# Kernel tuning notes

Hardware: AMD Instinct MI355X
Metric: run time of the kernel (lower is better)

## Reference

```python
import jax, jax.numpy as jnp
import numpy as np

EPS = 1e-5

def gelu(x):
    return jax.nn.gelu(x, approximate=False)

def conv1x1(x, w, b):
    # x: [B,C,H,W], w: [O,C], b: [O]
    return jnp.einsum('bchw,oc->bohw', x, w) + b[None, :, None, None]

def dwconv3(x, w, b):
    # depthwise 3x3, w: [C,1,3,3]
    C = x.shape[1]
    y = jax.lax.conv_general_dilated(x, w, (1, 1), 'SAME',
                                     feature_group_count=C,
                                     dimension_numbers=('NCHW', 'OIHW', 'NCHW'))
    return y + b[None, :, None, None]

def groupnorm(x, g, b):
    # GroupNorm(1, C): normalize over (C,H,W) per sample, per-channel affine
    m = x.mean(axis=(1, 2, 3), keepdims=True)
    v = x.var(axis=(1, 2, 3), keepdims=True)
    xn = (x - m) * jax.lax.rsqrt(v + EPS)
    return xn * g[None, :, None, None] + b[None, :, None, None]

@jax.custom_vjp
def spike(u):
    return (u > 0.0).astype(u.dtype)

def _spike_fwd(u):
    return spike(u), u

def _spike_bwd(u, g):
    # rectangular surrogate gradient of width 0.5 around the threshold
    return (g * (jnp.abs(u) < 0.5).astype(g.dtype),)

spike.defvjp(_spike_fwd, _spike_bwd)

def lif_along(x, tau, vth, axis):
    # leaky-integrate-fire recurrence along `axis` (H or W) treated as time
    xt = jnp.moveaxis(x, axis, 0)  # [T, ...]
    z = jnp.zeros_like(xt[0])
    def step(carry, x_t):
        u_prev, o_prev = carry
        u = x_t + tau * u_prev * (1.0 - o_prev)  # hard reset on spike
        o = spike(u - vth)
        return (u, o), o
    _, out = jax.lax.scan(step, (z, z), xt)
    return jnp.moveaxis(out, 0, axis)


def setup_inputs() -> dict:
    key = jax.random.key(0)
    ks = jax.random.split(key, 8)
    B, C, H, W = 64, 96, 56, 56
    Hd = 4 * C
    def w(k, shape, s=0.02):
        return jax.random.normal(k, shape, jnp.float32) * s
    f32 = jnp.float32
    return dict(
        x=jax.random.normal(ks[0], (B, C, H, W), f32),
        n1g=jnp.ones(C, f32), n1b=jnp.zeros(C, f32),
        c1w=w(ks[1], (C, C)), c1b=jnp.zeros(C, f32),
        g1g=jnp.ones(C, f32), g1b=jnp.zeros(C, f32),
        dww=w(ks[2], (C, 1, 3, 3)), dwb=jnp.zeros(C, f32),
        g2g=jnp.ones(C, f32), g2b=jnp.zeros(C, f32),
        tau1=jnp.array(0.25, f32), vth1=jnp.array(-1.0, f32),
        tau2=jnp.array(0.25, f32), vth2=jnp.array(-1.0, f32),
        c21w=w(ks[3], (C, C)), c21b=jnp.zeros(C, f32),
        c22w=w(ks[4], (C, C)), c22b=jnp.zeros(C, f32),
        g3g=jnp.ones(C, f32), g3b=jnp.zeros(C, f32),
        c3w=w(ks[5], (C, C)), c3b=jnp.zeros(C, f32),
        n2g=jnp.ones(C, f32), n2b=jnp.zeros(C, f32),
        f1w=w(ks[6], (Hd, C)), f1b=jnp.zeros(Hd, f32),
        f2w=w(ks[7], (C, Hd)), f2b=jnp.zeros(C, f32),
    )


def reference(x, n1g, n1b, c1w, c1b, g1g, g1b, dww, dwb, g2g, g2b,
              tau1, vth1, tau2, vth2, c21w, c21b, c22w, c22b,
              g3g, g3b, c3w, c3b, n2g, n2b, f1w, f1b, f2w, f2b):
    shortcut = x
    # LIF module
    h = groupnorm(x, n1g, n1b)                               # block norm1 (MyNorm)
    h = gelu(groupnorm(conv1x1(h, c1w, c1b), g1g, g1b))      # conv1 -> norm1 -> GELU
    h = gelu(groupnorm(dwconv3(h, dww, dwb), g2g, g2b))      # dw1 -> norm2 -> GELU
    x_lr = lif_along(h, tau1, vth1, axis=2)                  # LIF over H
    x_td = lif_along(h, tau2, vth2, axis=3)                  # LIF over W
    h = gelu(conv1x1(x_lr, c21w, c21b)) + gelu(conv1x1(x_td, c22w, c22b))
    h = conv1x1(groupnorm(h, g3g, g3b), c3w, c3b)            # norm3 -> conv3
    x = shortcut + h
    # MLP branch (1x1 convs)
    m = groupnorm(x, n2g, n2b)
    m = conv1x1(gelu(conv1x1(m, f1w, f1b)), f2w, f2b)
    return x + m
```

## Files before the change

kernel.cpp:

```cpp
#include <hip/hip_runtime.h>

#define BB 64
#define CC 96
#define HH 56
#define WW 56
#define HWSZ (HH*WW)
#define CHW (CC*HWSZ)
#define NTOT ((size_t)BB*CHW)
#define S_SPLIT 32
#define CHUNK (CHW/S_SPLIT)
#define HD 384
#define NP 104

typedef float f32x4  __attribute__((ext_vector_type(4)));
typedef short bf16x8 __attribute__((ext_vector_type(8)));
typedef unsigned short u16x4 __attribute__((ext_vector_type(4)));

__device__ __forceinline__ unsigned short f2bf(float f) {
    unsigned int u = __float_as_uint(f);
    u = (u + 0x7FFFu + ((u >> 16) & 1u)) >> 16;
    return (unsigned short)u;
}
__device__ __forceinline__ float bf2f(unsigned short u) {
    return __uint_as_float(((unsigned int)u) << 16);
}
__device__ __forceinline__ float gelu_t(float x) {
    float s = x*x;
    float q = __builtin_fmaf(s, 0.102943f, 2.3021953f) * x;
    float t = exp2f(q);
    float r = __builtin_amdgcn_rcpf(1.0f + t);
    return __builtin_fmaf(-x, r, x);
}
__device__ __forceinline__ bf16x8 ldfrag(const unsigned short* p) {
    return *reinterpret_cast<const bf16x8*>(p);
}

__global__ __launch_bounds__(256) void wconv(const float* __restrict__ c1w, const float* __restrict__ c21w,
        const float* __restrict__ c22w, const float* __restrict__ c3w,
        const float* __restrict__ f1w, const float* __restrict__ f2w,
        unsigned short* __restrict__ wbf) {
    int i = blockIdx.x*256 + threadIdx.x;
    int blk = i / 9216;
    int idx = i - blk*9216;
    int tm   = idx / 1536;
    int rem  = idx - tm*1536;
    int ks   = rem / 512;
    int rem2 = rem - ks*512;
    int lane = rem2 >> 3;
    int j    = rem2 & 7;
    int row = tm*16 + (lane & 15);
    int col = ks*32 + (lane >> 4)*8 + j;
    float v;
    if      (blk == 0) v = c1w [row*CC + col];
    else if (blk == 1) v = c21w[row*CC + col];
    else if (blk == 2) v = c22w[row*CC + col];
    else if (blk == 3) v = c3w [row*CC + col];
    else if (blk <  8) v = f1w[((blk-4)*CC + row)*CC + col];
    else               v = f2w[row*HD + (blk-8)*CC + col];
    wbf[i] = f2bf(v);
}

__global__ __launch_bounds__(256) void gn_partial(const float* __restrict__ in, float2* __restrict__ part) {
    int b = blockIdx.y, s = blockIdx.x;
    const float* p = in + (size_t)b*CHW + (size_t)s*CHUNK;
    float sum = 0.f, sq = 0.f;
    for (int i = threadIdx.x; i < CHUNK; i += 256) {
        float v = p[i];
        sum += v; sq += v*v;
    }
    for (int off = 32; off > 0; off >>= 1) {
        sum += __shfl_down(sum, off);
        sq  += __shfl_down(sq,  off);
    }
    __shared__ float2 red[4];
    int wid = threadIdx.x >> 6, lane = threadIdx.x & 63;
    if (lane == 0) red[wid] = make_float2(sum, sq);
    __syncthreads();
    if (threadIdx.x == 0) {
        for (int i = 1; i < 4; i++) { sum += red[i].x; sq += red[i].y; }
        part[b*S_SPLIT + s] = make_float2(sum, sq);
    }
}

template<int NPART>
__global__ void gn_final(const float2* __restrict__ part, float2* __restrict__ stats) {
    int b = threadIdx.x;
    if (b >= BB) return;
    float s = 0.f, q = 0.f;
    for (int i = 0; i < NPART; i++) { float2 v = part[b*NPART + i]; s += v.x; q += v.y; }
    float mean = s / (float)CHW;
    float var  = q / (float)CHW - mean*mean;
    stats[b] = make_float2(mean, rsqrtf(var + 1e-5f));
}

template<bool IN_BF, bool OUT_RES>
__global__ __launch_bounds__(256) void convk(const void* __restrict__ in_,
        const unsigned short* __restrict__ wbf, const float* __restrict__ bias,
        const float2* __restrict__ st_in, const float* __restrict__ gam, const float* __restrict__ bet,
        const float* __restrict__ res, void* __restrict__ out_, float2* __restrict__ part) {
    __shared__ unsigned short xs[128][NP];
    __shared__ float gml[CC], btl[CC];
    __shared__ float2 red[8];
    int tid = threadIdx.x;
    int b0 = blockIdx.y, b1 = b0 + 32;
    int hw0 = blockIdx.x * 64;
    if (tid < CC) { gml[tid] = gam[tid]; btl[tid] = bet[tid]; }
    float2 st0 = st_in[b0], st1 = st_in[b1];
    __syncthreads();
    int col = tid & 63;
    for (int c4 = (tid >> 6)*4; c4 < CC; c4 += 16) {
        unsigned int pk0[2], pk1[2];
        #pragma unroll
        for (int j = 0; j < 4; j++) {
            int c = c4 + j;
            size_t off0 = (size_t)b0*CHW + (size_t)c*HWSZ + hw0 + col;
            size_t off1 = (size_t)b1*CHW + (size_t)c*HWSZ + hw0 + col;
            float r0 = IN_BF ? bf2f(((const unsigned short*)in_)[off0]) : ((const float*)in_)[off0];
            float r1 = IN_BF ? bf2f(((const unsigned short*)in_)[off1]) : ((const float*)in_)[off1];
            float a0 = st0.y * gml[c], b0c = __builtin_fmaf(-st0.x, a0, btl[c]);
            float a1 = st1.y * gml[c], b1c = __builtin_fmaf(-st1.x, a1, btl[c]);
            unsigned short h0 = f2bf(__builtin_fmaf(r0, a0, b0c));
            unsigned short h1 = f2bf(__builtin_fmaf(r1, a1, b1c));
            if (j < 2) { if (j == 0) { pk0[0] = h0; pk1[0] = h1; } else { pk0[0] |= (unsigned int)h0 << 16; pk1[0] |= (unsigned int)h1 << 16; } }
            else       { if (j == 2) { pk0[1] = h0; pk1[1] = h1; } else { pk0[1] |= (unsigned int)h0 << 16; pk1[1] |= (unsigned int)h1 << 16; } }
        }
        *reinterpret_cast<uint2*>(&xs[col][c4])      = make_uint2(pk0[0], pk0[1]);
        *reinterpret_cast<uint2*>(&xs[64+col][c4])   = make_uint2(pk1[0], pk1[1]);
    }
    __syncthreads();
    int lane = tid & 63, wid = tid >> 6;
    int ln = lane & 15, k0 = (lane >> 4)*8, n0 = wid*16;
    const unsigned short* wl = wbf + lane*8;
    f32x4 a0[6], a1[6];
    #pragma unroll
    for (int t = 0; t < 6; t++) { a0[t] = (f32x4){0,0,0,0}; a1[t] = (f32x4){0,0,0,0}; }
    #pragma unroll
    for (int ks = 0; ks < 3; ks++) {
        bf16x8 bf0 = ldfrag(&xs[n0+ln][ks*32+k0]);
        bf16x8 bf1 = ldfrag(&xs[64+n0+ln][ks*32+k0]);
        #pragma unroll
        for (int tm = 0; tm < 6; tm++) {
            bf16x8 af = ldfrag(wl + (tm*3+ks)*512);
            a0[tm] = __builtin_amdgcn_mfma_f32_16x16x32_bf16(af, bf0, a0[tm], 0, 0, 0);
            a1[tm] = __builtin_amdgcn_mfma_f32_16x16x32_bf16(af, bf1, a1[tm], 0, 0, 0);
        }
    }
    int r0i = (lane >> 4)*4;
    size_t ob0 = (size_t)b0*CHW + hw0 + n0 + ln;
    size_t ob1 = (size_t)b1*CHW + hw0 + n0 + ln;
    float s0 = 0.f, q0 = 0.f, s1 = 0.f, q1 = 0.f;
    #pragma unroll
    for (int tm = 0; tm < 6; tm++) {
        #pragma unroll
        for (int r = 0; r < 4; r++) {
            int o = tm*16 + r0i + r;
            size_t i0 = ob0 + (size_t)o*HWSZ, i1 = ob1 + (size_t)o*HWSZ;
            float v0 = a0[tm][r] + bias[o];
            float v1 = a1[tm][r] + bias[o];
            if (OUT_RES) { v0 += res[i0]; v1 += res[i1];
                           ((float*)out_)[i0] = v0; ((float*)out_)[i1] = v1; }
            else         { ((unsigned short*)out_)[i0] = f2bf(v0); ((unsigned short*)out_)[i1] = f2bf(v1); }
            s0 += v0; q0 += v0*v0; s1 += v1; q1 += v1*v1;
        }
    }
    for (int off = 32; off > 0; off >>= 1) {
        s0 += __shfl_down(s0, off); q0 += __shfl_down(q0, off);
        s1 += __shfl_down(s1, off); q1 += __shfl_down(q1, off);
    }
    if (lane == 0) { red[wid] = make_float2(s0, q0); red[4+wid] = make_float2(s1, q1); }
    __syncthreads();
    if (tid == 0) {
        float S0=0,Q0=0,S1=0,Q1=0;
        for (int i = 0; i < 4; i++) { S0 += red[i].x; Q0 += red[i].y; S1 += red[4+i].x; Q1 += red[4+i].y; }
        part[b0*49 + blockIdx.x] = make_float2(S0, Q0);
        part[b1*49 + blockIdx.x] = make_float2(S1, Q1);
    }
}

__global__ __launch_bounds__(256) void dw_fused(const unsigned short* __restrict__ t1,
        const float* __restrict__ dww, const float* __restrict__ dwb,
        const float2* __restrict__ st_in, const float* __restrict__ gam, const float* __restrict__ bet,
        unsigned short* __restrict__ t2, float2* __restrict__ part) {
    __shared__ float tile[HH*57];
    __shared__ float2 red[4];
    int bc = blockIdx.x;
    int b = bc / CC, c = bc - b*CC;
    int tid = threadIdx.x;
    float2 st = st_in[b];
    float ga = gam[c]*st.y;
    float bb = __builtin_fmaf(-st.x, ga, bet[c]);
    const unsigned short* ip = t1 + (size_t)bc*HWSZ;
    for (int i = tid; i < HWSZ; i += 256) {
        float v = __builtin_fmaf(bf2f(ip[i]), ga, bb);
        tile[(i/WW)*57 + (i%WW)] = gelu_t(v);
    }
    __syncthreads();
    float w00=dww[c*9+0],w01=dww[c*9+1],w02=dww[c*9+2],
          w10=dww[c*9+3],w11=dww[c*9+4],w12=dww[c*9+5],
          w20=dww[c*9+6],w21=dww[c*9+7],w22=dww[c*9+8];
    float bs = dwb[c];
    unsigned short* op = t2 + (size_t)bc*HWSZ;
    float s = 0.f, q = 0.f;
    for (int i = tid; i < HWSZ; i += 256) {
        int h = i/WW, w_ = i - h*WW;
        float acc = bs;
        int up = h > 0, dn = h < HH-1, lf = w_ > 0, rt = w_ < WW-1;
        const float* rm = &tile[(h-1)*57 + w_];
        const float* r0p = &tile[h*57 + w_];
        const float* rp = &tile[(h+1)*57 + w_];
        if (up) { if (lf) acc += rm[-1]*w00; acc += rm[0]*w01; if (rt) acc += rm[1]*w02; }
        if (lf) acc += r0p[-1]*w10;
        acc += r0p[0]*w11;
        if (rt) acc += r0p[1]*w12;
        if (dn) { if (lf) acc += rp[-1]*w20; acc += rp[0]*w21; if (rt) acc += rp[1]*w22; }
        op[i] = f2bf(acc);
        s += acc; q += acc*acc;
    }
    for (int off = 32; off > 0; off >>= 1) { s += __shfl_down(s, off); q += __shfl_down(q, off); }
    int wid = tid >> 6, lane = tid & 63;
    if (lane == 0) red[wid] = make_float2(s, q);
    __syncthreads();
    if (tid == 0) {
        for (int i = 1; i < 4; i++) { s += red[i].x; q += red[i].y; }
        part[bc] = make_float2(s, q);
    }
}

__global__ __launch_bounds__(64) void lif_hw(const unsigned short* __restrict__ t2,
        unsigned short* __restrict__ xlr, unsigned short* __restrict__ xtd,
        const float2* __restrict__ st_in, const float* __restrict__ gam, const float* __restrict__ bet,
        const float* __restrict__ tau1p, const float* __restrict__ vth1p,
        const float* __restrict__ tau2p, const float* __restrict__ vth2p) {
    __shared__ float tile[HH*57];
    int bc = blockIdx.x;
    int b = bc / CC, c = bc - b*CC;
    int tid = threadIdx.x;
    float2 st = st_in[b];
    float ga = gam[c]*st.y;
    float bb = __builtin_fmaf(-st.x, ga, bet[c]);
    const unsigned short* ip = t2 + (size_t)bc*HWSZ;
    for (int i = tid; i < HWSZ/4; i += 64) {
        u16x4 v = *reinterpret_cast<const u16x4*>(ip + i*4);
        int h = i / 14;
        int w0 = (i - h*14)*4;
        float* tp = &tile[h*57 + w0];
        #pragma unroll
        for (int j = 0; j < 4; j++)
            tp[j] = gelu_t(__builtin_fmaf(bf2f((unsigned short)v[j]), ga, bb));
    }
    __syncthreads();
    const float tau1 = *tau1p, vth1 = *vth1p;
    if (tid < WW) {
        float u = 0.f, o = 0.f;
        unsigned short* op = xlr + (size_t)bc*HWSZ + tid;
        for (int h = 0; h < HH; h++) {
            float xv = tile[h*57 + tid];
            u = xv + tau1*u*(1.f - o);
            o = (u - vth1 > 0.f) ? 1.f : 0.f;
            op[h*WW] = (o != 0.f) ? (unsigned short)0x3F80 : (unsigned short)0;
        }
    }
    __syncthreads();
    const float tau2 = *tau2p, vth2 = *vth2p;
    if (tid < HH) {
        float u = 0.f, o = 0.f;
        int off = tid*57;
        for (int w_ = 0; w_ < WW; w_++) {
            float xv = tile[off + w_];
            u = xv + tau2*u*(1.f - o);
            o = (u - vth2 > 0.f) ? 1.f : 0.f;
            tile[off + w_] = o;
        }
    }
    __syncthreads();
    unsigned int* op32 = (unsigned int*)(xtd + (size_t)bc*HWSZ);
    for (int i = tid; i < HWSZ/2; i += 64) {
        int h = i / 28;
        int w0 = (i - h*28)*2;
        unsigned int lo = tile[h*57 + w0]     != 0.f ? 0x3F80u : 0u;
        unsigned int hi = tile[h*57 + w0 + 1] != 0.f ? 0x3F80u : 0u;
        op32[i] = lo | (hi << 16);
    }
}

__global__ __launch_bounds__(256) void dual_mfma(const unsigned short* __restrict__ xa_g, const unsigned short* __restrict__ xb_g,
        const unsigned short* __restrict__ w1bf, const float* __restrict__ b1,
        const unsigned short* __restrict__ w2bf, const float* __restrict__ b2,
        unsigned short* __restrict__ out, float2* __restrict__ part) {
    __shared__ unsigned short xa[64][NP];
    __shared__ unsigned short xb[64][NP];
    __shared__ float2 red[4];
    int tid = threadIdx.x;
    int b = blockIdx.y;
    int hw0 = blockIdx.x * 64;
    int col = tid & 63;
    const unsigned short* ap = xa_g + (size_t)b*CHW + hw0 + col;
    const unsigned short* bp = xb_g + (size_t)b*CHW + hw0 + col;
    for (int c4 = (tid >> 6)*4; c4 < CC; c4 += 16) {
        unsigned int pa0, pa1, pb0, pb1;
        unsigned short a0 = ap[(size_t)(c4+0)*HWSZ], a1v = ap[(size_t)(c4+1)*HWSZ];
        unsigned short a2 = ap[(size_t)(c4+2)*HWSZ], a3 = ap[(size_t)(c4+3)*HWSZ];
        unsigned short b0v = bp[(size_t)(c4+0)*HWSZ], b1v = bp[(size_t)(c4+1)*HWSZ];
        unsigned short b2v = bp[(size_t)(c4+2)*HWSZ], b3v = bp[(size_t)(c4+3)*HWSZ];
        pa0 = (unsigned int)a0 | ((unsigned int)a1v << 16);
        pa1 = (unsigned int)a2 | ((unsigned int)a3 << 16);
        pb0 = (unsigned int)b0v | ((unsigned int)b1v << 16);
        pb1 = (unsigned int)b2v | ((unsigned int)b3v << 16);
        *reinterpret_cast<uint2*>(&xa[col][c4]) = make_uint2(pa0, pa1);
        *reinterpret_cast<uint2*>(&xb[col][c4]) = make_uint2(pb0, pb1);
    }
    __syncthreads();
    int lane = tid & 63, wid = tid >> 6;
    int ln = lane & 15, k0 = (lane >> 4)*8, n0 = wid*16;
    const unsigned short* wl1 = w1bf + lane*8;
    const unsigned short* wl2 = w2bf + lane*8;
    f32x4 acc1[6], acc2[6];
    #pragma unroll
    for (int t = 0; t < 6; t++) { acc1[t] = (f32x4){0,0,0,0}; acc2[t] = (f32x4){0,0,0,0}; }
    #pragma unroll
    for (int ks = 0; ks < 3; ks++) {
        bf16x8 bfa = ldfrag(&xa[n0+ln][ks*32+k0]);
        bf16x8 bfb = ldfrag(&xb[n0+ln][ks*32+k0]);
        #pragma unroll
        for (int tm = 0; tm < 6; tm++) {
            bf16x8 af1 = ldfrag(wl1 + (tm*3+ks)*512);
            bf16x8 af2 = ldfrag(wl2 + (tm*3+ks)*512);
            acc1[tm] = __builtin_amdgcn_mfma_f32_16x16x32_bf16(af1, bfa, acc1[tm], 0, 0, 0);
            acc2[tm] = __builtin_amdgcn_mfma_f32_16x16x32_bf16(af2, bfb, acc2[tm], 0, 0, 0);
        }
    }
    int r0i = (lane >> 4)*4;
    size_t ob = (size_t)b*CHW + hw0 + n0 + ln;
    float s = 0.f, q = 0.f;
    #pragma unroll
    for (int tm = 0; tm < 6; tm++) {
        #pragma unroll
        for (int r = 0; r < 4; r++) {
            int o = tm*16 + r0i + r;
            float v = gelu_t(acc1[tm][r] + b1[o]) + gelu_t(acc2[tm][r] + b2[o]);
            out[ob + (size_t)o*HWSZ] = f2bf(v);
            s += v; q += v*v;
        }
    }
    for (int off = 32; off > 0; off >>= 1) { s += __shfl_down(s, off); q += __shfl_down(q, off); }
    if (lane == 0) red[wid] = make_float2(s, q);
    __syncthreads();
    if (tid == 0) {
        for (int i = 1; i < 4; i++) { s += red[i].x; q += red[i].y; }
        part[b*49 + blockIdx.x] = make_float2(s, q);
    }
}

__global__ __launch_bounds__(512, 4) void mlp_mfma(float* __restrict__ xio, const float2* __restrict__ st_in,
        const float* __restrict__ gam, const float* __restrict__ bet,
        const unsigned short* __restrict__ wbf, const float* __restrict__ b1, const float* __restrict__ b2) {
    __shared__ unsigned short xs[128][NP];
    __shared__ unsigned short mc[128][NP];
    __shared__ float gml[CC], btl[CC];
    int tid = threadIdx.x;
    int b0 = blockIdx.y, b1i = b0 + 32;
    int hw0 = blockIdx.x * 64;
    if (tid < CC) { gml[tid] = gam[tid]; btl[tid] = bet[tid]; }
    float2 st0 = st_in[b0], st1 = st_in[b1i];
    __syncthreads();
    {
        int col = tid & 63;
        int bsel0 = (tid >> 6) & 1;
        float2 st = bsel0 ? st1 : st0;
        size_t base = (size_t)(bsel0 ? b1i : b0)*CHW + hw0 + col;
        for (int c4 = (tid >> 7)*4; c4 < CC; c4 += 16) {
            unsigned int pk[2];
            #pragma unroll
            for (int j = 0; j < 4; j++) {
                int c = c4 + j;
                float rv = xio[base + (size_t)c*HWSZ];
                float a = st.y * gml[c];
                float bc = __builtin_fmaf(-st.x, a, btl[c]);
                unsigned short h = f2bf(__builtin_fmaf(rv, a, bc));
                if (j < 2) { if (j == 0) pk[0] = h; else pk[0] |= (unsigned int)h << 16; }
                else       { if (j == 2) pk[1] = h; else pk[1] |= (unsigned int)h << 16; }
            }
            *reinterpret_cast<uint2*>(&xs[bsel0*64 + col][c4]) = make_uint2(pk[0], pk[1]);
        }
    }
    __syncthreads();
    int lane = tid & 63, wv = tid >> 6;
    int mh = wv >> 2;
    int cg = wv & 3;
    int ln = lane & 15, k0 = (lane >> 4)*8;
    int r0i = (lane >> 4)*4;
    int xrow0 = cg*32 + ln;
    int xrow1 = xrow0 + 16;
    f32x4 ao[3][2];
    #pragma unroll
    for (int t = 0; t < 3; t++) { ao[t][0] = (f32x4){0,0,0,0}; ao[t][1] = (f32x4){0,0,0,0}; }
    for (int ch = 0; ch < 4; ch++) {
        const unsigned short* w1l = wbf + (4+ch)*9216 + mh*4608 + lane*8;
        const unsigned short* w2l = wbf + (8+ch)*9216 + mh*4608 + lane*8;
        f32x4 c1[3][2];
        #pragma unroll
        for (int t = 0; t < 3; t++) { c1[t][0] = (f32x4){0,0,0,0}; c1[t][1] = (f32x4){0,0,0,0}; }
        __builtin_amdgcn_s_setprio(1);
        #pragma unroll
        for (int ks = 0; ks < 3; ks++) {
            bf16x8 bfa = ldfrag(&xs[xrow0][ks*32+k0]);
            bf16x8 bfb = ldfrag(&xs[xrow1][ks*32+k0]);
            #pragma unroll
            for (int tm = 0; tm < 3; tm++) {
                bf16x8 af = ldfrag(w1l + (tm*3+ks)*512);
                c1[tm][0] = __builtin_amdgcn_mfma_f32_16x16x32_bf16(af, bfa, c1[tm][0], 0, 0, 0);
                c1[tm][1] = __builtin_amdgcn_mfma_f32_16x16x32_bf16(af, bfb, c1[tm][1], 0, 0, 0);
            }
        }
        __builtin_amdgcn_s_setprio(0);
        #pragma unroll
        for (int tm = 0; tm < 3; tm++) {
            int d0 = mh*48 + tm*16 + r0i;
            int dch = ch*CC + d0;
            unsigned short m0 = f2bf(gelu_t(c1[tm][0][0] + b1[dch+0]));
            unsigned short m1 = f2bf(gelu_t(c1[tm][0][1] + b1[dch+1]));
            unsigned short m2 = f2bf(gelu_t(c1[tm][0][2] + b1[dch+2]));
            unsigned short m3 = f2bf(gelu_t(c1[tm][0][3] + b1[dch+3]));
            *reinterpret_cast<uint2*>(&mc[xrow0][d0]) =
                make_uint2((unsigned int)m0 | ((unsigned int)m1 << 16),
                           (unsigned int)m2 | ((unsigned int)m3 << 16));
            unsigned short n0v = f2bf(gelu_t(c1[tm][1][0] + b1[dch+0]));
            unsigned short n1v = f2bf(gelu_t(c1[tm][1][1] + b1[dch+1]));
            unsigned short n2v = f2bf(gelu_t(c1[tm][1][2] + b1[dch+2]));
            unsigned short n3v = f2bf(gelu_t(c1[tm][1][3] + b1[dch+3]));
            *reinterpret_cast<uint2*>(&mc[xrow1][d0]) =
                make_uint2((unsigned int)n0v | ((unsigned int)n1v << 16),
                           (unsigned int)n2v | ((unsigned int)n3v << 16));
        }
        __syncthreads();
        __builtin_amdgcn_s_setprio(1);
        #pragma unroll
        for (int ks = 0; ks < 3; ks++) {
            bf16x8 bfa = ldfrag(&mc[xrow0][ks*32+k0]);
            bf16x8 bfb = ldfrag(&mc[xrow1][ks*32+k0]);
            #pragma unroll
            for (int tm = 0; tm < 3; tm++) {
                bf16x8 af = ldfrag(w2l + (tm*3+ks)*512);
                ao[tm][0] = __builtin_amdgcn_mfma_f32_16x16x32_bf16(af, bfa, ao[tm][0], 0, 0, 0);
                ao[tm][1] = __builtin_amdgcn_mfma_f32_16x16x32_bf16(af, bfb, ao[tm][1], 0, 0, 0);
            }
        }
        __builtin_amdgcn_s_setprio(0);
        __syncthreads();
    }
    int bsel = cg >> 1;
    size_t ob = (size_t)(bsel ? b1i : b0)*CHW + hw0 + (cg & 1)*32 + ln;
    #pragma unroll
    for (int tm = 0; tm < 3; tm++) {
        #pragma unroll
        for (int r = 0; r < 4; r++) {
            int o = mh*48 + tm*16 + r0i + r;
            size_t i0 = ob + (size_t)o*HWSZ;
            float bo = b2[o];
            xio[i0]      = xio[i0]      + bo + ao[tm][0][r];
            xio[i0 + 16] = xio[i0 + 16] + bo + ao[tm][1][r];
        }
    }
}

extern "C" void kernel_launch(void* const* d_in, const int* in_sizes, int n_in,
                              void* d_out, int out_size, void* d_ws, size_t ws_size,
                              hipStream_t stream) {
    (void)in_sizes; (void)n_in; (void)out_size; (void)ws_size;
    const float* x    = (const float*)d_in[0];
    const float* n1g  = (const float*)d_in[1];
    const float* n1b  = (const float*)d_in[2];
    const float* c1w  = (const float*)d_in[3];
    const float* c1b  = (const float*)d_in[4];
    const float* g1g  = (const float*)d_in[5];
    const float* g1b  = (const float*)d_in[6];
    const float* dww  = (const float*)d_in[7];
    const float* dwb  = (const float*)d_in[8];
    const float* g2g  = (const float*)d_in[9];
    const float* g2b  = (const float*)d_in[10];
    const float* tau1 = (const float*)d_in[11];
    const float* vth1 = (const float*)d_in[12];
    const float* tau2 = (const float*)d_in[13];
    const float* vth2 = (const float*)d_in[14];
    const float* c21w = (const float*)d_in[15];
    const float* c21b = (const float*)d_in[16];
    const float* c22w = (const float*)d_in[17];
    const float* c22b = (const float*)d_in[18];
    const float* g3g  = (const float*)d_in[19];
    const float* g3b  = (const float*)d_in[20];
    const float* c3w  = (const float*)d_in[21];
    const float* c3b  = (const float*)d_in[22];
    const float* n2g  = (const float*)d_in[23];
    const float* n2b  = (const float*)d_in[24];
    const float* f1w  = (const float*)d_in[25];
    const float* f1b  = (const float*)d_in[26];
    const float* f2w  = (const float*)d_in[27];
    const float* f2b  = (const float*)d_in[28];
    float* out = (float*)d_out;

    unsigned short* A   = (unsigned short*)d_ws;
    unsigned short* Bb  = A  + NTOT;
    unsigned short* Cc  = Bb + NTOT;
    unsigned short* WBF = Cc + NTOT;
    float2* part  = (float2*)(WBF + 110592);
    float2* stats = part + 64*96;
    float2* s_n1 = stats, * s_g1 = stats+64, * s_g2 = stats+128, * s_g3 = stats+192, * s_n2 = stats+256;

    const unsigned short* Wc1  = WBF;
    const unsigned short* Wc21 = WBF + 9216;
    const unsigned short* Wc22 = WBF + 18432;
    const unsigned short* Wc3  = WBF + 27648;

    dim3 gStat(S_SPLIT, BB);
    dim3 gPair(HWSZ/64, BB/2);
    dim3 gSing(HWSZ/64, BB);

    wconv<<<432,256,0,stream>>>(c1w, c21w, c22w, c3w, f1w, f2w, WBF);
    gn_partial<<<gStat,256,0,stream>>>(x, part);
    gn_final<S_SPLIT><<<1,64,0,stream>>>(part, s_n1);
    convk<false,false><<<gPair,256,0,stream>>>(x, Wc1, c1b, s_n1, n1g, n1b, nullptr, A, part);
    gn_final<49><<<1,64,0,stream>>>(part, s_g1);
    dw_fused<<<BB*CC,256,0,stream>>>(A, dww, dwb, s_g1, g1g, g1b, Bb, part);
    gn_final<CC><<<1,64,0,stream>>>(part, s_g2);
    lif_hw<<<BB*CC,64,0,stream>>>(Bb, A, Cc, s_g2, g2g, g2b, tau1, vth1, tau2, vth2);
    dual_mfma<<<gSing,256,0,stream>>>(A, Cc, Wc21, c21b, Wc22, c22b, Bb, part);
    gn_final<49><<<1,64,0,stream>>>(part, s_g3);
    convk<true,true><<<gPair,256,0,stream>>>(Bb, Wc3, c3b, s_g3, g3g, g3b, x, out, part);
    gn_final<49><<<1,64,0,stream>>>(part, s_n2);
    mlp_mfma<<<gPair,512,0,stream>>>(out, s_n2, n2g, n2b, WBF, f1b, f2b);
}
```

Before: 319.8 us.

## Fold groupnorm finalization into consumer kernels and rebalance MFMA wave tiling

```diff
diff --git a/kernel.cpp b/kernel.cpp
--- a/kernel.cpp
+++ b/kernel.cpp
@@ -33,6 +33,24 @@
 }
 __device__ __forceinline__ bf16x8 ldfrag(const unsigned short* p) {
     return *reinterpret_cast<const bf16x8*>(p);
+}
+template<int NPART>
+__device__ __forceinline__ float2 stats_from_parts(const float2* __restrict__ part, int b) {
+    int lane = threadIdx.x & 63;
+    float s = 0.f, q = 0.f;
+    for (int i = lane; i < NPART; i += 64) {
+        float2 v = part[b*NPART + i];
+        s += v.x; q += v.y;
+    }
+    #pragma unroll
+    for (int off = 32; off > 0; off >>= 1) {
+        s += __shfl_down(s, off);
+        q += __shfl_down(q, off);
+    }
+    s = __shfl(s, 0); q = __shfl(q, 0);
+    float mean = s / (float)CHW;
+    float var  = q / (float)CHW - mean*mean;
+    return make_float2(mean, rsqrtf(var + 1e-5f));
 }
 
 __global__ __launch_bounds__(256) void wconv(const float* __restrict__ c1w, const float* __restrict__ c21w,
@@ -62,12 +80,14 @@
 
 __global__ __launch_bounds__(256) void gn_partial(const float* __restrict__ in, float2* __restrict__ part) {
     int b = blockIdx.y, s = blockIdx.x;
-    const float* p = in + (size_t)b*CHW + (size_t)s*CHUNK;
+    const float4* p = (const float4*)(in + (size_t)b*CHW + (size_t)s*CHUNK);
     float sum = 0.f, sq = 0.f;
-    for (int i = threadIdx.x; i < CHUNK; i += 256) {
-        float v = p[i];
-        sum += v; sq += v*v;
-    }
+    for (int i = threadIdx.x; i < CHUNK/4; i += 256) {
+        float4 v = p[i];
+        sum += v.x+v.y+v.z+v.w;
+        sq  += v.x*v.x+v.y*v.y+v.z*v.z+v.w*v.w;
+    }
+    #pragma unroll
     for (int off = 32; off > 0; off >>= 1) {
         sum += __shfl_down(sum, off);
         sq  += __shfl_down(sq,  off);
@@ -82,30 +102,20 @@
     }
 }
 
-template<int NPART>
-__global__ void gn_final(const float2* __restrict__ part, float2* __restrict__ stats) {
-    int b = threadIdx.x;
-    if (b >= BB) return;
-    float s = 0.f, q = 0.f;
-    for (int i = 0; i < NPART; i++) { float2 v = part[b*NPART + i]; s += v.x; q += v.y; }
-    float mean = s / (float)CHW;
-    float var  = q / (float)CHW - mean*mean;
-    stats[b] = make_float2(mean, rsqrtf(var + 1e-5f));
-}
-
-template<bool IN_BF, bool OUT_RES>
+template<bool IN_BF, bool OUT_RES, int NPART>
 __global__ __launch_bounds__(256) void convk(const void* __restrict__ in_,
         const unsigned short* __restrict__ wbf, const float* __restrict__ bias,
-        const float2* __restrict__ st_in, const float* __restrict__ gam, const float* __restrict__ bet,
-        const float* __restrict__ res, void* __restrict__ out_, float2* __restrict__ part) {
+        const float2* __restrict__ part_in, const float* __restrict__ gam, const float* __restrict__ bet,
+        const float* __restrict__ res, void* __restrict__ out_, float2* __restrict__ part_out) {
     __shared__ unsigned short xs[128][NP];
     __shared__ float gml[CC], btl[CC];
-    __shared__ float2 red[8];
+    __shared__ float2 red[4];
     int tid = threadIdx.x;
     int b0 = blockIdx.y, b1 = b0 + 32;
     int hw0 = blockIdx.x * 64;
+    float2 st0 = stats_from_parts<NPART>(part_in, b0);
+    float2 st1 = stats_from_parts<NPART>(part_in, b1);
     if (tid < CC) { gml[tid] = gam[tid]; btl[tid] = bet[tid]; }
-    float2 st0 = st_in[b0], st1 = st_in[b1];
     __syncthreads();
     int col = tid & 63;
     for (int c4 = (tid >> 6)*4; c4 < CC; c4 += 16) {
@@ -128,65 +138,67 @@
         *reinterpret_cast<uint2*>(&xs[64+col][c4])   = make_uint2(pk1[0], pk1[1]);
     }
     __syncthreads();
-    int lane = tid & 63, wid = tid >> 6;
-    int ln = lane & 15, k0 = (lane >> 4)*8, n0 = wid*16;
-    const unsigned short* wl = wbf + lane*8;
-    f32x4 a0[6], a1[6];
-    #pragma unroll
-    for (int t = 0; t < 6; t++) { a0[t] = (f32x4){0,0,0,0}; a1[t] = (f32x4){0,0,0,0}; }
+    int lane = tid & 63, wv = tid >> 6;
+    int mh = wv >> 1, cg = wv & 1;
+    int ln = lane & 15, k0 = (lane >> 4)*8, r0i = (lane >> 4)*4;
+    const unsigned short* wl = wbf + mh*4608 + lane*8;
+    f32x4 acc[3][4];
+    #pragma unroll
+    for (int t = 0; t < 3; t++)
+        #pragma unroll
+        for (int x = 0; x < 4; x++) acc[t][x] = (f32x4){0,0,0,0};
+    __builtin_amdgcn_s_setprio(1);
     #pragma unroll
     for (int ks = 0; ks < 3; ks++) {
-        bf16x8 bf0 = ldfrag(&xs[n0+ln][ks*32+k0]);
-        bf16x8 bf1 = ldfrag(&xs[64+n0+ln][ks*32+k0]);
-        #pragma unroll
-        for (int tm = 0; tm < 6; tm++) {
+        bf16x8 bfr[4];
+        #pragma unroll
+        for (int xr = 0; xr < 4; xr++) bfr[xr] = ldfrag(&xs[cg*64 + xr*16 + ln][ks*32+k0]);
+        #pragma unroll
+        for (int tm = 0; tm < 3; tm++) {
             bf16x8 af = ldfrag(wl + (tm*3+ks)*512);
-            a0[tm] = __builtin_amdgcn_mfma_f32_16x16x32_bf16(af, bf0, a0[tm], 0, 0, 0);
-            a1[tm] = __builtin_amdgcn_mfma_f32_16x16x32_bf16(af, bf1, a1[tm], 0, 0, 0);
-        }
-    }
-    int r0i = (lane >> 4)*4;
-    size_t ob0 = (size_t)b0*CHW + hw0 + n0 + ln;
-    size_t ob1 = (size_t)b1*CHW + hw0 + n0 + ln;
-    float s0 = 0.f, q0 = 0.f, s1 = 0.f, q1 = 0.f;
-    #pragma unroll
-    for (int tm = 0; tm < 6; tm++) {
-        #pragma unroll
-        for (int r = 0; r < 4; r++) {
-            int o = tm*16 + r0i + r;
-            size_t i0 = ob0 + (size_t)o*HWSZ, i1 = ob1 + (size_t)o*HWSZ;
-            float v0 = a0[tm][r] + bias[o];
-            float v1 = a1[tm][r] + bias[o];
-            if (OUT_RES) { v0 += res[i0]; v1 += res[i1];
-                           ((float*)out_)[i0] = v0; ((float*)out_)[i1] = v1; }
-            else         { ((unsigned short*)out_)[i0] = f2bf(v0); ((unsigned short*)out_)[i1] = f2bf(v1); }
-            s0 += v0; q0 += v0*v0; s1 += v1; q1 += v1*v1;
-        }
-    }
-    for (int off = 32; off > 0; off >>= 1) {
-        s0 += __shfl_down(s0, off); q0 += __shfl_down(q0, off);
-        s1 += __shfl_down(s1, off); q1 += __shfl_down(q1, off);
-    }
-    if (lane == 0) { red[wid] = make_float2(s0, q0); red[4+wid] = make_float2(s1, q1); }
+            #pragma unroll
+            for (int xr = 0; xr < 4; xr++)
+                acc[tm][xr] = __builtin_amdgcn_mfma_f32_16x16x32_bf16(af, bfr[xr], acc[tm][xr], 0, 0, 0);
+        }
+    }
+    __builtin_amdgcn_s_setprio(0);
+    size_t obase = (size_t)(cg ? b1 : b0)*CHW + hw0;
+    float s = 0.f, q = 0.f;
+    #pragma unroll
+    for (int tm = 0; tm < 3; tm++) {
+        #pragma unroll
+        for (int xr = 0; xr < 4; xr++) {
+            #pragma unroll
+            for (int r = 0; r < 4; r++) {
+                int o = mh*48 + tm*16 + r0i + r;
+                size_t idx = obase + (size_t)o*HWSZ + xr*16 + ln;
+                float v = acc[tm][xr][r] + bias[o];
+                if (OUT_RES) { v += res[idx]; ((float*)out_)[idx] = v; }
+                else         { ((unsigned short*)out_)[idx] = f2bf(v); }
+                s += v; q += v*v;
+            }
+        }
+    }
+    #pragma unroll
+    for (int off = 32; off > 0; off >>= 1) { s += __shfl_down(s, off); q += __shfl_down(q, off); }
+    if (lane == 0) red[wv] = make_float2(s, q);
     __syncthreads();
     if (tid == 0) {
-        float S0=0,Q0=0,S1=0,Q1=0;
-        for (int i = 0; i < 4; i++) { S0 += red[i].x; Q0 += red[i].y; S1 += red[4+i].x; Q1 += red[4+i].y; }
-        part[b0*49 + blockIdx.x] = make_float2(S0, Q0);
-        part[b1*49 + blockIdx.x] = make_float2(S1, Q1);
+        part_out[b0*49 + blockIdx.x] = make_float2(red[0].x + red[2].x, red[0].y + red[2].y);
+        part_out[b1*49 + blockIdx.x] = make_float2(red[1].x + red[3].x, red[1].y + red[3].y);
     }
 }
 
 __global__ __launch_bounds__(256) void dw_fused(const unsigned short* __restrict__ t1,
         const float* __restrict__ dww, const float* __restrict__ dwb,
-        const float2* __restrict__ st_in, const float* __restrict__ gam, const float* __restrict__ bet,
-        unsigned short* __restrict__ t2, float2* __restrict__ part) {
+        const float2* __restrict__ part_in, const float* __restrict__ gam, const float* __restrict__ bet,
+        unsigned short* __restrict__ t2, float2* __restrict__ part_out) {
     __shared__ float tile[HH*57];
     __shared__ float2 red[4];
     int bc = blockIdx.x;
     int b = bc / CC, c = bc - b*CC;
     int tid = threadIdx.x;
-    float2 st = st_in[b];
+    float2 st = stats_from_parts<49>(part_in, b);
     float ga = gam[c]*st.y;
     float bb = __builtin_fmaf(-st.x, ga, bet[c]);
     const unsigned short* ip = t1 + (size_t)bc*HWSZ;
@@ -216,26 +228,27 @@
         op[i] = f2bf(acc);
         s += acc; q += acc*acc;
     }
+    #pragma unroll
     for (int off = 32; off > 0; off >>= 1) { s += __shfl_down(s, off); q += __shfl_down(q, off); }
     int wid = tid >> 6, lane = tid & 63;
     if (lane == 0) red[wid] = make_float2(s, q);
     __syncthreads();
     if (tid == 0) {
         for (int i = 1; i < 4; i++) { s += red[i].x; q += red[i].y; }
-        part[bc] = make_float2(s, q);
+        part_out[bc] = make_float2(s, q);
     }
 }
 
 __global__ __launch_bounds__(64) void lif_hw(const unsigned short* __restrict__ t2,
         unsigned short* __restrict__ xlr, unsigned short* __restrict__ xtd,
-        const float2* __restrict__ st_in, const float* __restrict__ gam, const float* __restrict__ bet,
+        const float2* __restrict__ part_in, const float* __restrict__ gam, const float* __restrict__ bet,
         const float* __restrict__ tau1p, const float* __restrict__ vth1p,
         const float* __restrict__ tau2p, const float* __restrict__ vth2p) {
     __shared__ float tile[HH*57];
     int bc = blockIdx.x;
     int b = bc / CC, c = bc - b*CC;
     int tid = threadIdx.x;
-    float2 st = st_in[b];
+    float2 st = stats_from_parts<96>(part_in, b);
     float ga = gam[c]*st.y;
     float bb = __builtin_fmaf(-st.x, ga, bet[c]);
     const unsigned short* ip = t2 + (size_t)bc*HWSZ;
@@ -286,7 +299,7 @@
 __global__ __launch_bounds__(256) void dual_mfma(const unsigned short* __restrict__ xa_g, const unsigned short* __restrict__ xb_g,
         const unsigned short* __restrict__ w1bf, const float* __restrict__ b1,
         const unsigned short* __restrict__ w2bf, const float* __restrict__ b2,
-        unsigned short* __restrict__ out, float2* __restrict__ part) {
+        unsigned short* __restrict__ out, float2* __restrict__ part_out) {
     __shared__ unsigned short xa[64][NP];
     __shared__ unsigned short xb[64][NP];
     __shared__ float2 red[4];
@@ -297,72 +310,80 @@
     const unsigned short* ap = xa_g + (size_t)b*CHW + hw0 + col;
     const unsigned short* bp = xb_g + (size_t)b*CHW + hw0 + col;
     for (int c4 = (tid >> 6)*4; c4 < CC; c4 += 16) {
-        unsigned int pa0, pa1, pb0, pb1;
         unsigned short a0 = ap[(size_t)(c4+0)*HWSZ], a1v = ap[(size_t)(c4+1)*HWSZ];
         unsigned short a2 = ap[(size_t)(c4+2)*HWSZ], a3 = ap[(size_t)(c4+3)*HWSZ];
         unsigned short b0v = bp[(size_t)(c4+0)*HWSZ], b1v = bp[(size_t)(c4+1)*HWSZ];
         unsigned short b2v = bp[(size_t)(c4+2)*HWSZ], b3v = bp[(size_t)(c4+3)*HWSZ];
-        pa0 = (unsigned int)a0 | ((unsigned int)a1v << 16);
-        pa1 = (unsigned int)a2 | ((unsigned int)a3 << 16);
-        pb0 = (unsigned int)b0v | ((unsigned int)b1v << 16);
-        pb1 = (unsigned int)b2v | ((unsigned int)b3v << 16);
-        *reinterpret_cast<uint2*>(&xa[col][c4]) = make_uint2(pa0, pa1);
-        *reinterpret_cast<uint2*>(&xb[col][c4]) = make_uint2(pb0, pb1);
-    }
-    __syncthreads();
-    int lane = tid & 63, wid = tid >> 6;
-    int ln = lane & 15, k0 = (lane >> 4)*8, n0 = wid*16;
-    const unsigned short* wl1 = w1bf + lane*8;
-    const unsigned short* wl2 = w2bf + lane*8;
-    f32x4 acc1[6], acc2[6];
-    #pragma unroll
-    for (int t = 0; t < 6; t++) { acc1[t] = (f32x4){0,0,0,0}; acc2[t] = (f32x4){0,0,0,0}; }
+        *reinterpret_cast<uint2*>(&xa[col][c4]) =
+            make_uint2((unsigned int)a0 | ((unsigned int)a1v << 16), (unsigned int)a2 | ((unsigned int)a3 << 16));
+        *reinterpret_cast<uint2*>(&xb[col][c4]) =
+            make_uint2((unsigned int)b0v | ((unsigned int)b1v << 16), (unsigned int)b2v | ((unsigned int)b3v << 16));
+    }
+    __syncthreads();
+    int lane = tid & 63, wv = tid >> 6;
+    int mh = wv >> 1, cg = wv & 1;
+    int ln = lane & 15, k0 = (lane >> 4)*8, r0i = (lane >> 4)*4;
+    const unsigned short* wl1 = w1bf + mh*4608 + lane*8;
+    const unsigned short* wl2 = w2bf + mh*4608 + lane*8;
+    f32x4 acc1[3][2], acc2[3][2];
+    #pragma unroll
+    for (int t = 0; t < 3; t++) {
+        acc1[t][0] = (f32x4){0,0,0,0}; acc1[t][1] = (f32x4){0,0,0,0};
+        acc2[t][0] = (f32x4){0,0,0,0}; acc2[t][1] = (f32x4){0,0,0,0};
+    }
+    __builtin_amdgcn_s_setprio(1);
     #pragma unroll
     for (int ks = 0; ks < 3; ks++) {
-        bf16x8 bfa = ldfrag(&xa[n0+ln][ks*32+k0]);
-        bf16x8 bfb = ldfrag(&xb[n0+ln][ks*32+k0]);
-        #pragma unroll
-        for (int tm = 0; tm < 6; tm++) {
+        bf16x8 bfa0 = ldfrag(&xa[cg*32 + ln][ks*32+k0]);
+        bf16x8 bfa1 = ldfrag(&xa[cg*32 + 16 + ln][ks*32+k0]);
+        bf16x8 bfb0 = ldfrag(&xb[cg*32 + ln][ks*32+k0]);
+        bf16x8 bfb1 = ldfrag(&xb[cg*32 + 16 + ln][ks*32+k0]);
+        #pragma unroll
+        for (int tm = 0; tm < 3; tm++) {
             bf16x8 af1 = ldfrag(wl1 + (tm*3+ks)*512);
             bf16x8 af2 = ldfrag(wl2 + (tm*3+ks)*512);
-            acc1[tm] = __builtin_amdgcn_mfma_f32_16x16x32_bf16(af1, bfa, acc1[tm], 0, 0, 0);
-            acc2[tm] = __builtin_amdgcn_mfma_f32_16x16x32_bf16(af2, bfb, acc2[tm], 0, 0, 0);
-        }
-    }
-    int r0i = (lane >> 4)*4;
-    size_t ob = (size_t)b*CHW + hw0 + n0 + ln;
+            acc1[tm][0] = __builtin_amdgcn_mfma_f32_16x16x32_bf16(af1, bfa0, acc1[tm][0], 0, 0, 0);
+            acc1[tm][1] = __builtin_amdgcn_mfma_f32_16x16x32_bf16(af1, bfa1, acc1[tm][1], 0, 0, 0);
+            acc2[tm][0] = __builtin_amdgcn_mfma_f32_16x16x32_bf16(af2, bfb0, acc2[tm][0], 0, 0, 0);
+            acc2[tm][1] = __builtin_amdgcn_mfma_f32_16x16x32_bf16(af2, bfb1, acc2[tm][1], 0, 0, 0);
+        }
+    }
+    __builtin_amdgcn_s_setprio(0);
+    size_t ob = (size_t)b*CHW + hw0;
     float s = 0.f, q = 0.f;
     #pragma unroll
-    for (int tm = 0; tm < 6; tm++) {
-        #pragma unroll
-        for (int r = 0; r < 4; r++) {
-            int o = tm*16 + r0i + r;
-            float v = gelu_t(acc1[tm][r] + b1[o]) + gelu_t(acc2[tm][r] + b2[o]);
-            out[ob + (size_t)o*HWSZ] = f2bf(v);
-            s += v; q += v*v;
-        }
-    }
+    for (int tm = 0; tm < 3; tm++) {
+        #pragma unroll
+        for (int xr = 0; xr < 2; xr++) {
+            #pragma unroll
+            for (int r = 0; r < 4; r++) {
+                int o = mh*48 + tm*16 + r0i + r;
+                float v = gelu_t(acc1[tm][xr][r] + b1[o]) + gelu_t(acc2[tm][xr][r] + b2[o]);
+                out[ob + (size_t)o*HWSZ + cg*32 + xr*16 + ln] = f2bf(v);
+                s += v; q += v*v;
+            }
+        }
+    }
+    #pragma unroll
     for (int off = 32; off > 0; off >>= 1) { s += __shfl_down(s, off); q += __shfl_down(q, off); }
-    if (lane == 0) red[wid] = make_float2(s, q);
+    if (lane == 0) red[wv] = make_float2(s, q);
     __syncthreads();
     if (tid == 0) {
         for (int i = 1; i < 4; i++) { s += red[i].x; q += red[i].y; }
-        part[b*49 + blockIdx.x] = make_float2(s, q);
-    }
-}
-
-__global__ __launch_bounds__(512, 4) void mlp_mfma(float* __restrict__ xio, const float2* __restrict__ st_in,
+        part_out[b*49 + blockIdx.x] = make_float2(s, q);
+    }
+}
+
+__global__ __launch_bounds__(512, 6) void mlp_mfma(float* __restrict__ xio, const float2* __restrict__ part_in,
         const float* __restrict__ gam, const float* __restrict__ bet,
         const unsigned short* __restrict__ wbf, const float* __restrict__ b1, const float* __restrict__ b2) {
     __shared__ unsigned short xs[128][NP];
     __shared__ unsigned short mc[128][NP];
-    __shared__ float gml[CC], btl[CC];
     int tid = threadIdx.x;
     int b0 = blockIdx.y, b1i = b0 + 32;
     int hw0 = blockIdx.x * 64;
-    if (tid < CC) { gml[tid] = gam[tid]; btl[tid] = bet[tid]; }
-    float2 st0 = st_in[b0], st1 = st_in[b1i];
-    __syncthreads();
+    float2 st0 = stats_from_parts<49>(part_in, b0);
+    float2 st1 = stats_from_parts<49>(part_in, b1i);
     {
         int col = tid & 63;
         int bsel0 = (tid >> 6) & 1;
@@ -374,8 +395,8 @@
             for (int j = 0; j < 4; j++) {
                 int c = c4 + j;
                 float rv = xio[base + (size_t)c*HWSZ];
-                float a = st.y * gml[c];
-                float bc = __builtin_fmaf(-st.x, a, btl[c]);
+                float a = st.y * gam[c];
+                float bc = __builtin_fmaf(-st.x, a, bet[c]);
                 unsigned short h = f2bf(__builtin_fmaf(rv, a, bc));
                 if (j < 2) { if (j == 0) pk[0] = h; else pk[0] |= (unsigned int)h << 16; }
                 else       { if (j == 2) pk[1] = h; else pk[1] |= (unsigned int)h << 16; }
@@ -502,9 +523,11 @@
     unsigned short* Bb  = A  + NTOT;
     unsigned short* Cc  = Bb + NTOT;
     unsigned short* WBF = Cc + NTOT;
-    float2* part  = (float2*)(WBF + 110592);
-    float2* stats = part + 64*96;
-    float2* s_n1 = stats, * s_g1 = stats+64, * s_g2 = stats+128, * s_g3 = stats+192, * s_n2 = stats+256;
+    float2* part0 = (float2*)(WBF + 110592);
+    float2* part1 = part0 + 64*32;
+    float2* part2 = part1 + 64*49;
+    float2* part3 = part2 + 64*96;
+    float2* part4 = part3 + 64*49;
 
     const unsigned short* Wc1  = WBF;
     const unsigned short* Wc21 = WBF + 9216;
@@ -516,16 +539,11 @@
     dim3 gSing(HWSZ/64, BB);
 
     wconv<<<432,256,0,stream>>>(c1w, c21w, c22w, c3w, f1w, f2w, WBF);
-    gn_partial<<<gStat,256,0,stream>>>(x, part);
-    gn_final<S_SPLIT><<<1,64,0,stream>>>(part, s_n1);
-    convk<false,false><<<gPair,256,0,stream>>>(x, Wc1, c1b, s_n1, n1g, n1b, nullptr, A, part);
-    gn_final<49><<<1,64,0,stream>>>(part, s_g1);
-    dw_fused<<<BB*CC,256,0,stream>>>(A, dww, dwb, s_g1, g1g, g1b, Bb, part);
-    gn_final<CC><<<1,64,0,stream>>>(part, s_g2);
-    lif_hw<<<BB*CC,64,0,stream>>>(Bb, A, Cc, s_g2, g2g, g2b, tau1, vth1, tau2, vth2);
-    dual_mfma<<<gSing,256,0,stream>>>(A, Cc, Wc21, c21b, Wc22, c22b, Bb, part);
-    gn_final<49><<<1,64,0,stream>>>(part, s_g3);
-    convk<true,true><<<gPair,256,0,stream>>>(Bb, Wc3, c3b, s_g3, g3g, g3b, x, out, part);
-    gn_final<49><<<1,64,0,stream>>>(part, s_n2);
-    mlp_mfma<<<gPair,512,0,stream>>>(out, s_n2, n2g, n2b, WBF, f1b, f2b);
-}
+    gn_partial<<<gStat,256,0,stream>>>(x, part0);
+    convk<false,false,S_SPLIT><<<gPair,256,0,stream>>>(x, Wc1, c1b, part0, n1g, n1b, nullptr, A, part1);
+    dw_fused<<<BB*CC,256,0,stream>>>(A, dww, dwb, part1, g1g, g1b, Bb, part2);
+    lif_hw<<<BB*CC,64,0,stream>>>(Bb, A, Cc, part2, g2g, g2b, tau1, vth1, tau2, vth2);
+    dual_mfma<<<gSing,256,0,stream>>>(A, Cc, Wc21, c21b, Wc22, c22b, Bb, part3);
+    convk<true,true,49><<<gPair,256,0,stream>>>(Bb, Wc3, c3b, part3, g3g, g3b, x, out, part4);
+    mlp_mfma<<<gPair,512,0,stream>>>(out, part4, n2g, n2b, WBF, f1b, f2b);
+}
```

Result: slower. 336.2 us (+5.1%).
